# Kernel tuning notes

Measured on AMD Instinct MI355X. Metric: run time of the kernel, lower is better.

## Reference

```python
import jax, jax.numpy as jnp
import numpy as np

B, F_IN, D_SKETCH, N_CLASSES = 256, 2048, 8192, 14951


def setup_inputs() -> dict:
    key = jax.random.key(0)
    k = jax.random.split(key, 7)
    x = jax.random.normal(k[0], (B, F_IN), dtype=jnp.float32)
    # count-sketch hash indices (fixed buffers)
    h1 = jax.random.randint(k[1], (F_IN,), 0, D_SKETCH, dtype=jnp.int32)
    h2 = jax.random.randint(k[2], (F_IN,), 0, D_SKETCH, dtype=jnp.int32)
    # Rademacher signs in {-1,+1} (fixed buffers)
    s1 = (jax.random.randint(k[3], (F_IN,), 0, 2) * 2 - 1).astype(jnp.float32)
    s2 = (jax.random.randint(k[4], (F_IN,), 0, 2) * 2 - 1).astype(jnp.float32)
    # Linear layer params
    W = jax.random.normal(k[5], (N_CLASSES, D_SKETCH), dtype=jnp.float32) * 0.01
    b = jnp.zeros((N_CLASSES,), dtype=jnp.float32)
    return {"x": x, "h1": h1, "h2": h2, "s1": s1, "s2": s2, "W": W, "b": b}


def _count_sketch(x, h, s, d):
    # scatter-add signed features into d buckets: sk[b, h[i]] += s[i] * x[b, i]
    return jnp.zeros((x.shape[0], d), dtype=x.dtype).at[:, h].add(x * s)


def reference(x, h1, h2, s1, s2, W, b):
    d = W.shape[1]
    sk1 = _count_sketch(x, h1, s1, d)
    sk2 = _count_sketch(x, h2, s2, d)
    # compact bilinear pooling: circular convolution of sketches via FFT
    prod = jnp.fft.rfft(sk1, axis=-1) * jnp.fft.rfft(sk2, axis=-1)
    cbp = jnp.fft.irfft(prod, n=d, axis=-1)  # [B, D]
    return cbp @ W.T + b  # [B, N_CLASSES]
```

## Files before the change

### kernel.cpp

```cpp
#include <hip/hip_runtime.h>
#include <hip/hip_bf16.h>

#define BATCH 256
#define FIN 2048
#define D 8192
#define NC 14951

typedef __attribute__((ext_vector_type(8))) short short8;
typedef __attribute__((ext_vector_type(4))) float f32x4;

__device__ __forceinline__ unsigned short f2bf(float f) {
    unsigned u = __float_as_uint(f);
    u += 0x7FFFu + ((u >> 16) & 1u);
    return (unsigned short)(u >> 16);
}
__device__ __forceinline__ float bf2f(unsigned short h) {
    return __uint_as_float(((unsigned)h) << 16);
}

#define PADI(i) ((i) + ((i) >> 3))

__device__ __forceinline__ float2 cmul(float2 a, float2 b) {
    return make_float2(a.x * b.x - a.y * b.y, a.x * b.y + a.y * b.x);
}

template<int SGN>
__device__ __forceinline__ void radix8_stage(const float2* __restrict__ src,
                                             float2* __restrict__ dst,
                                             int ns, int tid)
{
    float2 z[8];
#pragma unroll
    for (int k = 0; k < 8; ++k) z[k] = src[PADI(tid + k * 1024)];

    const int j = tid & (ns - 1);
    const float ang = (float)SGN * 6.28318530717958647692f * ((float)j / (float)(8 * ns));
    float sn, cs;
    __sincosf(ang, &sn, &cs);
    float2 w1 = make_float2(cs, sn);
    float2 w2 = cmul(w1, w1), w3 = cmul(w2, w1), w4 = cmul(w2, w2);
    float2 w5 = cmul(w4, w1), w6 = cmul(w4, w2), w7 = cmul(w4, w3);

    float2 u0 = z[0],           u1 = cmul(z[1], w1), u2 = cmul(z[2], w2), u3 = cmul(z[3], w3);
    float2 u4 = cmul(z[4], w4), u5 = cmul(z[5], w5), u6 = cmul(z[6], w6), u7 = cmul(z[7], w7);

    const float sg = (float)SGN;
    float2 t0 = make_float2(u0.x + u4.x, u0.y + u4.y);
    float2 t1 = make_float2(u0.x - u4.x, u0.y - u4.y);
    float2 t2 = make_float2(u2.x + u6.x, u2.y + u6.y);
    float2 t3 = make_float2(u2.x - u6.x, u2.y - u6.y);
    float2 E0 = make_float2(t0.x + t2.x, t0.y + t2.y);
    float2 E2 = make_float2(t0.x - t2.x, t0.y - t2.y);
    float2 E1 = make_float2(t1.x - sg * t3.y, t1.y + sg * t3.x);
    float2 E3 = make_float2(t1.x + sg * t3.y, t1.y - sg * t3.x);
    float2 s0 = make_float2(u1.x + u5.x, u1.y + u5.y);
    float2 s1 = make_float2(u1.x - u5.x, u1.y - u5.y);
    float2 s2 = make_float2(u3.x + u7.x, u3.y + u7.y);
    float2 s3 = make_float2(u3.x - u7.x, u3.y - u7.y);
    float2 O0 = make_float2(s0.x + s2.x, s0.y + s2.y);
    float2 O2 = make_float2(s0.x - s2.x, s0.y - s2.y);
    float2 O1 = make_float2(s1.x - sg * s3.y, s1.y + sg * s3.x);
    float2 O3 = make_float2(s1.x + sg * s3.y, s1.y - sg * s3.x);
    const float C8 = 0.70710678118654752440f;
    float2 P1 = make_float2(C8 * (O1.x - sg * O1.y), C8 * (O1.y + sg * O1.x));
    float2 P2 = make_float2(-sg * O2.y, sg * O2.x);
    float2 P3 = make_float2(C8 * (-O3.x - sg * O3.y), C8 * (sg * O3.x - O3.y));

    const int base = 8 * tid - 7 * j;
    dst[PADI(base + 0 * ns)] = make_float2(E0.x + O0.x, E0.y + O0.y);
    dst[PADI(base + 1 * ns)] = make_float2(E1.x + P1.x, E1.y + P1.y);
    dst[PADI(base + 2 * ns)] = make_float2(E2.x + P2.x, E2.y + P2.y);
    dst[PADI(base + 3 * ns)] = make_float2(E3.x + P3.x, E3.y + P3.y);
    dst[PADI(base + 4 * ns)] = make_float2(E0.x - O0.x, E0.y - O0.y);
    dst[PADI(base + 5 * ns)] = make_float2(E1.x - P1.x, E1.y - P1.y);
    dst[PADI(base + 6 * ns)] = make_float2(E2.x - P2.x, E2.y - P2.y);
    dst[PADI(base + 7 * ns)] = make_float2(E3.x - P3.x, E3.y - P3.y);
}

template<int SGN>
__device__ __forceinline__ void radix2_final(const float2* __restrict__ src,
                                             float2* __restrict__ dst, int tid)
{
#pragma unroll
    for (int it = 0; it < 4; ++it) {
        int i = tid + it * 1024;
        float2 a = src[PADI(i)];
        float2 c = src[PADI(i + 4096)];
        float ang = (float)SGN * 6.28318530717958647692f * ((float)i * (1.0f / 8192.0f));
        float sn, cs;
        __sincosf(ang, &sn, &cs);
        float2 wc = make_float2(cs * c.x - sn * c.y, cs * c.y + sn * c.x);
        dst[PADI(i)]        = make_float2(a.x + wc.x, a.y + wc.y);
        dst[PADI(i + 4096)] = make_float2(a.x - wc.x, a.y - wc.y);
    }
}

__global__ __launch_bounds__(1024) void cbp_kernel(
    const float* __restrict__ x, const int* __restrict__ h1, const int* __restrict__ h2,
    const float* __restrict__ s1, const float* __restrict__ s2,
    unsigned short* __restrict__ Ah, unsigned short* __restrict__ Al)
{
    __shared__ float2 bufA[9216];
    __shared__ float2 bufB[9216];
    const int b = blockIdx.x;
    const int tid = threadIdx.x;

    for (int i = tid; i < 9216; i += 1024) bufA[i] = make_float2(0.f, 0.f);
    __syncthreads();

    const float* xrow = x + (size_t)b * FIN;
#pragma unroll
    for (int it = 0; it < 2; ++it) {
        int i = tid + it * 1024;
        float v = xrow[i];
        atomicAdd(&bufA[PADI(h1[i])].x, s1[i] * v);
        atomicAdd(&bufA[PADI(h2[i])].y, s2[i] * v);
    }
    __syncthreads();

    radix8_stage<-1>(bufA, bufB, 1, tid);   __syncthreads();
    radix8_stage<-1>(bufB, bufA, 8, tid);   __syncthreads();
    radix8_stage<-1>(bufA, bufB, 64, tid);  __syncthreads();
    radix8_stage<-1>(bufB, bufA, 512, tid); __syncthreads();
    radix2_final<-1>(bufA, bufB, tid);      __syncthreads();

#pragma unroll
    for (int it = 0; it < 8; ++it) {
        int k = tid + it * 1024;
        float2 zk = bufB[PADI(k)];
        float2 zm = bufB[PADI((8192 - k) & 8191)];
        float f1x = 0.5f * (zk.x + zm.x);
        float f1y = 0.5f * (zk.y - zm.y);
        float gx  = 0.5f * (zk.x - zm.x);
        float gy  = 0.5f * (zk.y + zm.y);
        float f2x = gy, f2y = -gx;
        bufA[PADI(k)] = make_float2(f1x * f2x - f1y * f2y, f1x * f2y + f1y * f2x);
    }
    __syncthreads();

    radix8_stage<1>(bufA, bufB, 1, tid);   __syncthreads();
    radix8_stage<1>(bufB, bufA, 8, tid);   __syncthreads();
    radix8_stage<1>(bufA, bufB, 64, tid);  __syncthreads();
    radix8_stage<1>(bufB, bufA, 512, tid); __syncthreads();
    radix2_final<1>(bufA, bufB, tid);      __syncthreads();

    const float invD = 1.0f / 8192.0f;
    unsigned short* ah = Ah + (size_t)b * D;
    unsigned short* al = Al + (size_t)b * D;
#pragma unroll
    for (int it = 0; it < 8; ++it) {
        int t = tid + it * 1024;
        float v = bufB[PADI(t)].x * invD;
        unsigned short h = f2bf(v);
        unsigned short l = f2bf(v - bf2f(h));
        ah[t] = h;
        al[t] = l;
    }
}

#define BM 128
#define BN 64
#define KS 64

__global__ __launch_bounds__(512, 4) void gemm_kernel(
    const unsigned short* __restrict__ Ah, const unsigned short* __restrict__ Al,
    const float* __restrict__ W, const float* __restrict__ bias,
    float* __restrict__ out)
{
    __shared__ __align__(16) unsigned short lA[2][2][BM * KS];
    __shared__ __align__(16) unsigned short lB[2][BN * KS];

    const int tid = threadIdx.x;
    const int wave = tid >> 6;
    const int lane = tid & 63;
    const int wm = wave >> 1;
    const int wn = wave & 1;
    const int r16 = lane & 15;
    const int q8  = (lane >> 4) * 8;

    const int orig = blockIdx.x;
    const int xcd = orig & 7, idx = orig >> 3;
    const int wg = (xcd < 4 ? xcd * 59 : 236 + (xcd - 4) * 58) + idx;
    const int n0 = (wg >> 1) * BN;
    const int m0 = (wg & 1) * BM;

    const int bn = tid >> 3;
    const int bk8 = (tid & 7) * 8;

    f32x4 acc[2][2];
#pragma unroll
    for (int i = 0; i < 2; ++i)
#pragma unroll
        for (int jj = 0; jj < 2; ++jj) acc[i][jj] = (f32x4){0.f, 0.f, 0.f, 0.f};

    float4 pbw0, pbw1;

    auto LOADW = [&](int k0) {
        const int n = n0 + bn;
        if (n < NC) {
            const float4* gw = reinterpret_cast<const float4*>(W + (size_t)n * D + k0 + bk8);
            pbw0 = gw[0];
            pbw1 = gw[1];
        } else {
            pbw0 = make_float4(0.f, 0.f, 0.f, 0.f);
            pbw1 = make_float4(0.f, 0.f, 0.f, 0.f);
        }
    };

    auto STOREB = [&]() {
        float pf[8] = {pbw0.x, pbw0.y, pbw0.z, pbw0.w, pbw1.x, pbw1.y, pbw1.z, pbw1.w};
        unsigned short h[8], l[8];
#pragma unroll
        for (int jj = 0; jj < 8; ++jj) {
            h[jj] = f2bf(pf[jj]);
            l[jj] = f2bf(pf[jj] - bf2f(h[jj]));
        }
        uint4 hv, lv;
        hv.x = (unsigned)h[0] | ((unsigned)h[1] << 16);
        hv.y = (unsigned)h[2] | ((unsigned)h[3] << 16);
        hv.z = (unsigned)h[4] | ((unsigned)h[5] << 16);
        hv.w = (unsigned)h[6] | ((unsigned)h[7] << 16);
        lv.x = (unsigned)l[0] | ((unsigned)l[1] << 16);
        lv.y = (unsigned)l[2] | ((unsigned)l[3] << 16);
        lv.z = (unsigned)l[4] | ((unsigned)l[5] << 16);
        lv.w = (unsigned)l[6] | ((unsigned)l[7] << 16);
        const int byteoff = (bn * 128 + (tid & 7) * 16) ^ ((bn & 7) << 4);
        *reinterpret_cast<uint4*>((char*)&lB[0][0] + byteoff) = hv;
        *reinterpret_cast<uint4*>((char*)&lB[1][0] + byteoff) = lv;
    };

    auto STAGE_A = [&](int k0, int buf) {
#pragma unroll
        for (int p = 0; p < 2; ++p) {
            const unsigned short* gp = p ? Al : Ah;
#pragma unroll
            for (int c = 0; c < 2; ++c) {
                const int T = (wave * 2 + c) * 64 + lane;
                const int row = T >> 3;
                const int lcol = (T & 7) ^ (row & 7);
                const unsigned short* src = gp + (size_t)(m0 + row) * D + k0 + lcol * 8;
                char* dst = (char*)&lA[buf][p][0] + (wave * 2 + c) * 1024;
                __builtin_amdgcn_global_load_lds(
                    (const __attribute__((address_space(1))) void*)src,
                    (__attribute__((address_space(3))) void*)dst, 16, 0, 0);
            }
        }
    };

    auto COMPUTE = [&](int buf) {
#pragma unroll
        for (int ksub = 0; ksub < 2; ++ksub) {
            const int keb = (ksub * 32 + q8) * 2;
            short8 a_hi[2], a_lo[2], b_hi[2], b_lo[2];
#pragma unroll
            for (int rb = 0; rb < 2; ++rb) {
                const int row = wm * 32 + rb * 16 + r16;
                const int bo = (row * 128 + keb) ^ ((row & 7) << 4);
                a_hi[rb] = *reinterpret_cast<const short8*>((const char*)&lA[buf][0][0] + bo);
                a_lo[rb] = *reinterpret_cast<const short8*>((const char*)&lA[buf][1][0] + bo);
            }
#pragma unroll
            for (int nb = 0; nb < 2; ++nb) {
                const int row = wn * 32 + nb * 16 + r16;
                const int bo = (row * 128 + keb) ^ ((row & 7) << 4);
                b_hi[nb] = *reinterpret_cast<const short8*>((const char*)&lB[0][0] + bo);
                b_lo[nb] = *reinterpret_cast<const short8*>((const char*)&lB[1][0] + bo);
            }
#pragma unroll
            for (int rb = 0; rb < 2; ++rb)
#pragma unroll
                for (int nb = 0; nb < 2; ++nb) {
                    acc[rb][nb] = __builtin_amdgcn_mfma_f32_16x16x32_bf16(a_hi[rb], b_hi[nb], acc[rb][nb], 0, 0, 0);
                    acc[rb][nb] = __builtin_amdgcn_mfma_f32_16x16x32_bf16(a_hi[rb], b_lo[nb], acc[rb][nb], 0, 0, 0);
                    acc[rb][nb] = __builtin_amdgcn_mfma_f32_16x16x32_bf16(a_lo[rb], b_hi[nb], acc[rb][nb], 0, 0, 0);
                }
        }
    };

    LOADW(0);
    STAGE_A(0, 0);
    int buf = 0;
    for (int k0 = 0; k0 < D; k0 += KS) {
        __syncthreads();
        STOREB();
        __syncthreads();
        if (k0 + KS < D) {
            STAGE_A(k0 + KS, buf ^ 1);
            LOADW(k0 + KS);
        }
        COMPUTE(buf);
        buf ^= 1;
    }

    const int rq = (lane >> 4) * 4;
#pragma unroll
    for (int nb = 0; nb < 2; ++nb) {
        const int nc = n0 + wn * 32 + nb * 16 + r16;
        if (nc < NC) {
            const float bv = bias[nc];
#pragma unroll
            for (int rb = 0; rb < 2; ++rb)
#pragma unroll
                for (int r = 0; r < 4; ++r) {
                    const int m = m0 + wm * 32 + rb * 16 + rq + r;
                    out[(size_t)m * NC + nc] = acc[rb][nb][r] + bv;
                }
        }
    }
}

extern "C" void kernel_launch(void* const* d_in, const int* in_sizes, int n_in,
                              void* d_out, int out_size, void* d_ws, size_t ws_size,
                              hipStream_t stream) {
    (void)in_sizes; (void)n_in; (void)out_size;
    const float* x  = (const float*)d_in[0];
    const int*   h1 = (const int*)d_in[1];
    const int*   h2 = (const int*)d_in[2];
    const float* s1 = (const float*)d_in[3];
    const float* s2 = (const float*)d_in[4];
    const float* W  = (const float*)d_in[5];
    const float* bias = (const float*)d_in[6];
    float* out = (float*)d_out;

    const size_t A_BYTES = (size_t)BATCH * D * sizeof(unsigned short);
    if (ws_size < 2 * A_BYTES) return;

    unsigned short* Ah = (unsigned short*)d_ws;
    unsigned short* Al = (unsigned short*)((char*)d_ws + A_BYTES);

    cbp_kernel<<<dim3(BATCH), dim3(1024), 0, stream>>>(x, h1, h2, s1, s2, Ah, Al);
    const int nblocks = ((NC + BN - 1) / BN) * 2;
    gemm_kernel<<<dim3(nblocks), dim3(512), 0, stream>>>(Ah, Al, W, bias, out);
}
```

Baseline: 784.1 us.

## Split-K GEMM with larger N tiles, single-bf16 W, and atomic accumulation

Reworks the GEMM: the N tile grows to 128, K is split in half across workgroups, and results are combined with atomicAdd into an output pre-filled with bias by a new kernel. W is now rounded to a single bf16 with hardware pack-convert instead of a hi/lo split, which cuts MFMAs per tile from three to two and removes the LDS traffic for W's low half. The main loop is software-pipelined with explicit vmcnt/lgkmcnt waits and raw barriers. In exchange, W loses precision, the output becomes nondeterministic through float atomics, and correctness now depends on hand-placed wait counts.

Result: no change. 787.6 us (+0.5%).

```diff
diff --git a/kernel.cpp b/kernel.cpp
--- a/kernel.cpp
+++ b/kernel.cpp
@@ -22,6 +22,14 @@
 
 __device__ __forceinline__ float2 cmul(float2 a, float2 b) {
     return make_float2(a.x * b.x - a.y * b.y, a.x * b.y + a.y * b.x);
+}
+
+__global__ __launch_bounds__(1024) void bias_fill_kernel(
+    const float* __restrict__ bias, float* __restrict__ out)
+{
+    const int m = blockIdx.x;
+    float* row = out + (size_t)m * NC;
+    for (int n = threadIdx.x; n < NC; n += 1024) row[n] = bias[n];
 }
 
 template<int SGN>
@@ -158,17 +166,21 @@
     }
 }
 
-#define BM 128
-#define BN 64
-#define KS 64
+#define BMT 128
+#define BNT 128
+#define KS 32
+#define KHALF 4096
+
+#define VMCNT4() asm volatile("s_waitcnt vmcnt(4)" ::: "memory")
+#define VMCNT0() asm volatile("s_waitcnt vmcnt(0)" ::: "memory")
+#define LGKM0()  asm volatile("s_waitcnt lgkmcnt(0)" ::: "memory")
 
 __global__ __launch_bounds__(512, 4) void gemm_kernel(
     const unsigned short* __restrict__ Ah, const unsigned short* __restrict__ Al,
-    const float* __restrict__ W, const float* __restrict__ bias,
-    float* __restrict__ out)
-{
-    __shared__ __align__(16) unsigned short lA[2][2][BM * KS];
-    __shared__ __align__(16) unsigned short lB[2][BN * KS];
+    const float* __restrict__ W, float* __restrict__ out)
+{
+    __shared__ __align__(16) unsigned short lA[2][2][BMT * KS];
+    __shared__ __align__(16) unsigned short lB[2][BNT * KS];
 
     const int tid = threadIdx.x;
     const int wave = tid >> 6;
@@ -176,134 +188,129 @@
     const int wm = wave >> 1;
     const int wn = wave & 1;
     const int r16 = lane & 15;
-    const int q8  = (lane >> 4) * 8;
+    const int hi16 = (lane >> 4) * 16;
 
     const int orig = blockIdx.x;
     const int xcd = orig & 7, idx = orig >> 3;
     const int wg = (xcd < 4 ? xcd * 59 : 236 + (xcd - 4) * 58) + idx;
-    const int n0 = (wg >> 1) * BN;
-    const int m0 = (wg & 1) * BM;
-
-    const int bn = tid >> 3;
-    const int bk8 = (tid & 7) * 8;
-
-    f32x4 acc[2][2];
+    const int nt = wg >> 2;
+    const int mh = (wg >> 1) & 1;
+    const int kh = wg & 1;
+    const int n0 = nt * BNT;
+    const int m0 = mh * BMT;
+    const int kb = kh * KHALF;
+
+    const int srow = tid >> 2;
+    const int sc   = tid & 3;
+
+    f32x4 acc[2][4];
 #pragma unroll
     for (int i = 0; i < 2; ++i)
 #pragma unroll
-        for (int jj = 0; jj < 2; ++jj) acc[i][jj] = (f32x4){0.f, 0.f, 0.f, 0.f};
-
-    float4 pbw0, pbw1;
-
-    auto LOADW = [&](int k0) {
-        const int n = n0 + bn;
-        if (n < NC) {
-            const float4* gw = reinterpret_cast<const float4*>(W + (size_t)n * D + k0 + bk8);
-            pbw0 = gw[0];
-            pbw1 = gw[1];
-        } else {
-            pbw0 = make_float4(0.f, 0.f, 0.f, 0.f);
-            pbw1 = make_float4(0.f, 0.f, 0.f, 0.f);
+        for (int j = 0; j < 4; ++j) acc[i][j] = (f32x4){0.f, 0.f, 0.f, 0.f};
+
+    const int nW = (n0 + srow < NC) ? (n0 + srow) : (NC - 1);
+    const float* wsrc = W + (size_t)nW * D + kb + sc * 8;
+
+    const unsigned short* asrcH = Ah + (size_t)(m0 + srow) * D + kb + sc * 8;
+    const unsigned short* asrcL = Al + (size_t)(m0 + srow) * D + kb + sc * 8;
+
+    float4 wr0a, wr0b, wr1a, wr1b;
+
+    auto LOADW = [&](int kt, float4& a, float4& b) {
+        const float4* gw = reinterpret_cast<const float4*>(wsrc + kt * KS);
+        a = gw[0];
+        b = gw[1];
+    };
+
+    auto STAGE_A = [&](int kt, int buf) {
+        char* dstH = (char*)&lA[buf][0][0] + wave * 1024;
+        char* dstL = (char*)&lA[buf][1][0] + wave * 1024;
+        __builtin_amdgcn_global_load_lds(
+            (const __attribute__((address_space(1))) void*)(asrcH + kt * KS),
+            (__attribute__((address_space(3))) void*)dstH, 16, 0, 0);
+        __builtin_amdgcn_global_load_lds(
+            (const __attribute__((address_space(1))) void*)(asrcL + kt * KS),
+            (__attribute__((address_space(3))) void*)dstL, 16, 0, 0);
+    };
+
+    auto STOREB = [&](const float4& a, const float4& b, int buf) {
+        unsigned r0, r1, r2, r3;
+        asm("v_cvt_pk_bf16_f32 %0, %1, %2" : "=v"(r0) : "v"(a.x), "v"(a.y));
+        asm("v_cvt_pk_bf16_f32 %0, %1, %2" : "=v"(r1) : "v"(a.z), "v"(a.w));
+        asm("v_cvt_pk_bf16_f32 %0, %1, %2" : "=v"(r2) : "v"(b.x), "v"(b.y));
+        asm("v_cvt_pk_bf16_f32 %0, %1, %2" : "=v"(r3) : "v"(b.z), "v"(b.w));
+        uint4 v; v.x = r0; v.y = r1; v.z = r2; v.w = r3;
+        *reinterpret_cast<uint4*>((char*)&lB[buf][0] + srow * 64 + sc * 16) = v;
+    };
+
+    auto COMPUTE = [&](int buf) {
+        short8 a_hi[2], a_lo[2], bf[4];
+#pragma unroll
+        for (int rb = 0; rb < 2; ++rb) {
+            const int bo = (wm * 32 + rb * 16 + r16) * 64 + hi16;
+            a_hi[rb] = *reinterpret_cast<const short8*>((const char*)&lA[buf][0][0] + bo);
+            a_lo[rb] = *reinterpret_cast<const short8*>((const char*)&lA[buf][1][0] + bo);
         }
+#pragma unroll
+        for (int nb = 0; nb < 4; ++nb) {
+            const int bo = (wn * 64 + nb * 16 + r16) * 64 + hi16;
+            bf[nb] = *reinterpret_cast<const short8*>((const char*)&lB[buf][0] + bo);
+        }
+#pragma unroll
+        for (int rb = 0; rb < 2; ++rb)
+#pragma unroll
+            for (int nb = 0; nb < 4; ++nb) {
+                acc[rb][nb] = __builtin_amdgcn_mfma_f32_16x16x32_bf16(a_hi[rb], bf[nb], acc[rb][nb], 0, 0, 0);
+                acc[rb][nb] = __builtin_amdgcn_mfma_f32_16x16x32_bf16(a_lo[rb], bf[nb], acc[rb][nb], 0, 0, 0);
+            }
     };
 
-    auto STOREB = [&]() {
-        float pf[8] = {pbw0.x, pbw0.y, pbw0.z, pbw0.w, pbw1.x, pbw1.y, pbw1.z, pbw1.w};
-        unsigned short h[8], l[8];
-#pragma unroll
-        for (int jj = 0; jj < 8; ++jj) {
-            h[jj] = f2bf(pf[jj]);
-            l[jj] = f2bf(pf[jj] - bf2f(h[jj]));
-        }
-        uint4 hv, lv;
-        hv.x = (unsigned)h[0] | ((unsigned)h[1] << 16);
-        hv.y = (unsigned)h[2] | ((unsigned)h[3] << 16);
-        hv.z = (unsigned)h[4] | ((unsigned)h[5] << 16);
-        hv.w = (unsigned)h[6] | ((unsigned)h[7] << 16);
-        lv.x = (unsigned)l[0] | ((unsigned)l[1] << 16);
-        lv.y = (unsigned)l[2] | ((unsigned)l[3] << 16);
-        lv.z = (unsigned)l[4] | ((unsigned)l[5] << 16);
-        lv.w = (unsigned)l[6] | ((unsigned)l[7] << 16);
-        const int byteoff = (bn * 128 + (tid & 7) * 16) ^ ((bn & 7) << 4);
-        *reinterpret_cast<uint4*>((char*)&lB[0][0] + byteoff) = hv;
-        *reinterpret_cast<uint4*>((char*)&lB[1][0] + byteoff) = lv;
-    };
-
-    auto STAGE_A = [&](int k0, int buf) {
-#pragma unroll
-        for (int p = 0; p < 2; ++p) {
-            const unsigned short* gp = p ? Al : Ah;
-#pragma unroll
-            for (int c = 0; c < 2; ++c) {
-                const int T = (wave * 2 + c) * 64 + lane;
-                const int row = T >> 3;
-                const int lcol = (T & 7) ^ (row & 7);
-                const unsigned short* src = gp + (size_t)(m0 + row) * D + k0 + lcol * 8;
-                char* dst = (char*)&lA[buf][p][0] + (wave * 2 + c) * 1024;
-                __builtin_amdgcn_global_load_lds(
-                    (const __attribute__((address_space(1))) void*)src,
-                    (__attribute__((address_space(3))) void*)dst, 16, 0, 0);
-            }
-        }
-    };
-
-    auto COMPUTE = [&](int buf) {
-#pragma unroll
-        for (int ksub = 0; ksub < 2; ++ksub) {
-            const int keb = (ksub * 32 + q8) * 2;
-            short8 a_hi[2], a_lo[2], b_hi[2], b_lo[2];
-#pragma unroll
-            for (int rb = 0; rb < 2; ++rb) {
-                const int row = wm * 32 + rb * 16 + r16;
-                const int bo = (row * 128 + keb) ^ ((row & 7) << 4);
-                a_hi[rb] = *reinterpret_cast<const short8*>((const char*)&lA[buf][0][0] + bo);
-                a_lo[rb] = *reinterpret_cast<const short8*>((const char*)&lA[buf][1][0] + bo);
-            }
-#pragma unroll
-            for (int nb = 0; nb < 2; ++nb) {
-                const int row = wn * 32 + nb * 16 + r16;
-                const int bo = (row * 128 + keb) ^ ((row & 7) << 4);
-                b_hi[nb] = *reinterpret_cast<const short8*>((const char*)&lB[0][0] + bo);
-                b_lo[nb] = *reinterpret_cast<const short8*>((const char*)&lB[1][0] + bo);
-            }
-#pragma unroll
-            for (int rb = 0; rb < 2; ++rb)
-#pragma unroll
-                for (int nb = 0; nb < 2; ++nb) {
-                    acc[rb][nb] = __builtin_amdgcn_mfma_f32_16x16x32_bf16(a_hi[rb], b_hi[nb], acc[rb][nb], 0, 0, 0);
-                    acc[rb][nb] = __builtin_amdgcn_mfma_f32_16x16x32_bf16(a_hi[rb], b_lo[nb], acc[rb][nb], 0, 0, 0);
-                    acc[rb][nb] = __builtin_amdgcn_mfma_f32_16x16x32_bf16(a_lo[rb], b_hi[nb], acc[rb][nb], 0, 0, 0);
-                }
-        }
-    };
-
-    LOADW(0);
+    LOADW(0, wr0a, wr0b);
     STAGE_A(0, 0);
-    int buf = 0;
-    for (int k0 = 0; k0 < D; k0 += KS) {
-        __syncthreads();
-        STOREB();
-        __syncthreads();
-        if (k0 + KS < D) {
-            STAGE_A(k0 + KS, buf ^ 1);
-            LOADW(k0 + KS);
-        }
-        COMPUTE(buf);
-        buf ^= 1;
-    }
+    STOREB(wr0a, wr0b, 0);
+    LOADW(1, wr0a, wr0b);
+    LGKM0();
+    __builtin_amdgcn_s_barrier();
+
+#define ITER(K, RDYA, RDYB, FLYA, FLYB)                                    \
+    {                                                                      \
+        STAGE_A((K) + 1, ((K) + 1) & 1);                                   \
+        LOADW((K) + 2, FLYA, FLYB);                                        \
+        VMCNT4();                           \
+        COMPUTE((K) & 1);                                                  \
+        STOREB(RDYA, RDYB, ((K) + 1) & 1);                                 \
+        LGKM0();                                                           \
+        __builtin_amdgcn_s_barrier();                                      \
+    }
+
+    for (int kp = 0; kp < 63; ++kp) {
+        const int k = kp * 2;
+        ITER(k,     wr0a, wr0b, wr1a, wr1b);
+        ITER(k + 1, wr1a, wr1b, wr0a, wr0b);
+    }
+
+    STAGE_A(127, 1);
+    VMCNT4();
+    COMPUTE(0);
+    STOREB(wr0a, wr0b, 1);
+    LGKM0();
+    __builtin_amdgcn_s_barrier();
+
+    VMCNT0();
+    COMPUTE(1);
 
     const int rq = (lane >> 4) * 4;
 #pragma unroll
-    for (int nb = 0; nb < 2; ++nb) {
-        const int nc = n0 + wn * 32 + nb * 16 + r16;
+    for (int nb = 0; nb < 4; ++nb) {
+        const int nc = n0 + wn * 64 + nb * 16 + r16;
         if (nc < NC) {
-            const float bv = bias[nc];
 #pragma unroll
             for (int rb = 0; rb < 2; ++rb)
 #pragma unroll
                 for (int r = 0; r < 4; ++r) {
                     const int m = m0 + wm * 32 + rb * 16 + rq + r;
-                    out[(size_t)m * NC + nc] = acc[rb][nb][r] + bv;
+                    atomicAdd(&out[(size_t)m * NC + nc], acc[rb][nb][r]);
                 }
         }
     }
@@ -325,10 +332,10 @@
     const size_t A_BYTES = (size_t)BATCH * D * sizeof(unsigned short);
     if (ws_size < 2 * A_BYTES) return;
 
-    unsigned short* Ah = (unsigned short*)d_ws;
-    unsigned short* Al = (unsigned short*)((char*)d_ws + A_BYTES);
-
-    cbp_kernel<<<dim3(BATCH), dim3(1024), 0, stream>>>(x, h1, h2, s1, s2, Ah, Al);
-    const int nblocks = ((NC + BN - 1) / BN) * 2;
-    gemm_kernel<<<dim3(nblocks), dim3(512), 0, stream>>>(Ah, Al, W, bias, out);
-}
+    unsigned short* Ahp = (unsigned short*)d_ws;
+    unsigned short* Alp = (unsigned short*)((char*)d_ws + A_BYTES);
+
+    bias_fill_kernel<<<dim3(BATCH), dim3(1024), 0, stream>>>(bias, out);
+    cbp_kernel<<<dim3(BATCH), dim3(1024), 0, stream>>>(x, h1, h2, s1, s2, Ahp, Alp);
+    gemm_kernel<<<dim3(468), dim3(512), 0, stream>>>(Ahp, Alp, W, out);
+}
```
